# Kernel tuning notes

Hardware: AMD Instinct MI355X
Metric: run time of the kernel (lower is better)

## Reference

```python
import jax, jax.numpy as jnp
import numpy as np

NUM_MESHES = 8
NUM_FACES = 16384
NUM_NEIGHBOR = 3
SAMPLES_PER_NEIGHBOR = 8
NUM_SAMPLES = NUM_NEIGHBOR * SAMPLES_PER_NEIGHBOR  # 24
NUM_KERNEL = 64


def setup_inputs() -> dict:
    key = jax.random.key(0)
    ks = jax.random.split(key, 8)
    centers = jax.random.normal(ks[0], (NUM_MESHES, NUM_FACES, 3), dtype=jnp.float32)
    ring_n = jax.random.randint(ks[1], (NUM_MESHES, NUM_FACES, NUM_NEIGHBOR), 0, NUM_FACES)
    neighbor_corners = jax.random.normal(ks[2], (NUM_MESHES, NUM_FACES, NUM_NEIGHBOR, 3, 3), dtype=jnp.float32)
    # AlphaBetaGamma.initialize(): barycentric weights from r1, r2
    r1 = jax.random.uniform(ks[3], (NUM_FACES, NUM_SAMPLES), dtype=jnp.float32)
    r2 = jax.random.uniform(ks[4], (NUM_FACES, NUM_SAMPLES), dtype=jnp.float32)
    r1_sqrt = jnp.sqrt(r1)
    alpha = 1.0 - r1_sqrt
    beta = r1_sqrt * (1.0 - r2)
    gamma = r1_sqrt * r2
    W = jax.random.normal(ks[5], (NUM_KERNEL, 3), dtype=jnp.float32) * 0.1
    b = jnp.zeros((NUM_KERNEL,), dtype=jnp.float32)
    return {"centers": centers, "ring_n": ring_n, "neighbor_corners": neighbor_corners,
            "alpha": alpha, "beta": beta, "gamma": gamma, "W": W, "b": b}


def reference(centers, ring_n, neighbor_corners, alpha, beta, gamma, W, b):
    # Uniform neighbor resampling: tile each neighbor SAMPLES_PER_NEIGHBOR times
    # (torch.cat([neighbor_corners] * freq, dim=2))
    rs_nc = jnp.concatenate([neighbor_corners] * SAMPLES_PER_NEIGHBOR, axis=2)  # [M,F,S,3,3]
    c1, c2, c3 = rs_nc[:, :, :, 0, :], rs_nc[:, :, :, 1, :], rs_nc[:, :, :, 2, :]
    # barycentric surface points on neighbor faces: [M,F,S,3]
    a = alpha[None, :, :, None]
    bt = beta[None, :, :, None]
    g = gamma[None, :, :, None]
    points = a * c1 + bt * c2 + g * c3
    # geodesic direction vectors from face center to surface points
    dirs = points - centers[:, :, None, :]  # [M,F,S,3]
    # per-point kernel response, ReLU, then max over samples
    fea = jax.nn.relu(jnp.einsum('mfsc,kc->mfsk', dirs, W) + b)  # [M,F,S,K]
    out = jnp.max(fea, axis=2)  # [M,F,K]
    return out
```

## Files before the change

### kernel.cpp

```cpp
#include <hip/hip_runtime.h>


#define NM 8
#define NF 16384
#define NK 64

__global__ __launch_bounds__(256) void conv_surface_kernel(
    const float* __restrict__ centers,
    const float* __restrict__ nc,
    const float* __restrict__ beta,
    const float* __restrict__ gammav,
    const float* __restrict__ W,
    const float* __restrict__ b,
    float* __restrict__ out)
{
    const int lane = threadIdx.x & 63;
    const int wav  = __builtin_amdgcn_readfirstlane((int)(threadIdx.x >> 6));
    const int f    = blockIdx.x * 4 + wav;

    const float w0 = W[lane * 3 + 0];
    const float w1 = W[lane * 3 + 1];
    const float w2 = W[lane * 3 + 2];
    const float bk = b[lane];

    const float* __restrict__ bp = beta   + (size_t)f * 24;
    const float* __restrict__ gp = gammav + (size_t)f * 24;
    float bs[24], gs[24];
#pragma unroll
    for (int s = 0; s < 24; ++s) { bs[s] = bp[s]; gs[s] = gp[s]; }

#pragma unroll 2
    for (int m = 0; m < NM; ++m) {
        const size_t gidx = (size_t)m * NF + f;

        const float* __restrict__ cp = centers + gidx * 3;
        const float cdot = cp[0] * w0 + cp[1] * w1 + cp[2] * w2;

        const float* __restrict__ tp = nc + gidx * 27;
        float mx = -3.4e38f;
#pragma unroll
        for (int n = 0; n < 3; ++n) {
            const float* __restrict__ t = tp + n * 9;
            const float a1 = t[0] * w0 + t[1] * w1 + t[2] * w2;
            const float a2 = t[3] * w0 + t[4] * w1 + t[5] * w2;
            const float a3 = t[6] * w0 + t[7] * w1 + t[8] * w2;
            const float e2 = a2 - a1;
            const float e3 = a3 - a1;

            float v[8];
#pragma unroll
            for (int j = 0; j < 8; ++j) {
                const int s = n + 3 * j;
                v[j] = fmaf(bs[s], e2, fmaf(gs[s], e3, a1));
            }
            const float m0 = fmaxf(fmaxf(v[0], v[1]), fmaxf(v[2], v[3]));
            const float m1 = fmaxf(fmaxf(v[4], v[5]), fmaxf(v[6], v[7]));
            mx = fmaxf(mx, fmaxf(m0, m1));
        }

        out[gidx * NK + lane] = fmaxf(mx - cdot + bk, 0.0f);
    }
}

extern "C" void kernel_launch(void* const* d_in, const int* in_sizes, int n_in,
                              void* d_out, int out_size, void* d_ws, size_t ws_size,
                              hipStream_t stream) {
    const float* centers = (const float*)d_in[0];
    const float* nc      = (const float*)d_in[2];
    const float* beta    = (const float*)d_in[4];
    const float* gammav  = (const float*)d_in[5];
    const float* W       = (const float*)d_in[6];
    const float* b       = (const float*)d_in[7];
    float* out = (float*)d_out;

    dim3 grid(NF / 4), block(256);
    hipLaunchKernelGGL(conv_surface_kernel, grid, block, 0, stream,
                       centers, nc, beta, gammav, W, b, out);
}
```

Baseline: 36.66 us.

## Interchange mesh and neighbor loops to batch loads across all meshes

Swaps the loop order so the outer loop runs over the three neighbors and the inner loop over all eight meshes. For each neighbor, the triangle corners of every mesh are loaded together before compute, which raises memory-level parallelism. Only eight beta/gamma values per neighbor are held at a time instead of all 24, and launch bounds now request four blocks per CU. Stores are deferred to the end and need eight accumulators plus a 72-float staging array, which raises register pressure against the occupancy hint and risks spills.

```diff
diff --git a/kernel.cpp b/kernel.cpp
--- a/kernel.cpp
+++ b/kernel.cpp
@@ -5,7 +5,7 @@
 #define NF 16384
 #define NK 64
 
-__global__ __launch_bounds__(256) void conv_surface_kernel(
+__global__ __launch_bounds__(256, 4) void conv_surface_kernel(
     const float* __restrict__ centers,
     const float* __restrict__ nc,
     const float* __restrict__ beta,
@@ -23,43 +23,58 @@
     const float w2 = W[lane * 3 + 2];
     const float bk = b[lane];
 
-    const float* __restrict__ bp = beta   + (size_t)f * 24;
-    const float* __restrict__ gp = gammav + (size_t)f * 24;
-    float bs[24], gs[24];
+    float cdot[NM], mx[NM];
 #pragma unroll
-    for (int s = 0; s < 24; ++s) { bs[s] = bp[s]; gs[s] = gp[s]; }
+    for (int m = 0; m < NM; ++m) {
+        const float* __restrict__ cp = centers + ((size_t)m * NF + f) * 3;
+        cdot[m] = cp[0] * w0 + cp[1] * w1 + cp[2] * w2;
+        mx[m]   = -3.4e38f;
+    }
 
-#pragma unroll 2
-    for (int m = 0; m < NM; ++m) {
-        const size_t gidx = (size_t)m * NF + f;
+#pragma unroll
+    for (int n = 0; n < 3; ++n) {
+        float bn[8], gn[8];
+#pragma unroll
+        for (int j = 0; j < 8; ++j) {
+            bn[j] = beta  [(size_t)f * 24 + n + 3 * j];
+            gn[j] = gammav[(size_t)f * 24 + n + 3 * j];
+        }
 
-        const float* __restrict__ cp = centers + gidx * 3;
-        const float cdot = cp[0] * w0 + cp[1] * w1 + cp[2] * w2;
+        float ta[NM][9];
+#pragma unroll
+        for (int m = 0; m < NM; ++m) {
+            const float* __restrict__ t = nc + ((size_t)m * NF + f) * 27 + n * 9;
+#pragma unroll
+            for (int e = 0; e < 9; ++e) ta[m][e] = t[e];
+        }
 
-        const float* __restrict__ tp = nc + gidx * 27;
-        float mx = -3.4e38f;
 #pragma unroll
-        for (int n = 0; n < 3; ++n) {
-            const float* __restrict__ t = tp + n * 9;
-            const float a1 = t[0] * w0 + t[1] * w1 + t[2] * w2;
-            const float a2 = t[3] * w0 + t[4] * w1 + t[5] * w2;
-            const float a3 = t[6] * w0 + t[7] * w1 + t[8] * w2;
+        for (int m = 0; m < NM; ++m) {
+            const float a1 = ta[m][0] * w0 + ta[m][1] * w1 + ta[m][2] * w2;
+            const float a2 = ta[m][3] * w0 + ta[m][4] * w1 + ta[m][5] * w2;
+            const float a3 = ta[m][6] * w0 + ta[m][7] * w1 + ta[m][8] * w2;
             const float e2 = a2 - a1;
             const float e3 = a3 - a1;
 
-            float v[8];
+            const float v0 = fmaf(bn[0], e2, fmaf(gn[0], e3, a1));
+            const float v1 = fmaf(bn[1], e2, fmaf(gn[1], e3, a1));
+            const float v2 = fmaf(bn[2], e2, fmaf(gn[2], e3, a1));
+            const float v3 = fmaf(bn[3], e2, fmaf(gn[3], e3, a1));
+            const float v4 = fmaf(bn[4], e2, fmaf(gn[4], e3, a1));
+            const float v5 = fmaf(bn[5], e2, fmaf(gn[5], e3, a1));
+            const float v6 = fmaf(bn[6], e2, fmaf(gn[6], e3, a1));
+            const float v7 = fmaf(bn[7], e2, fmaf(gn[7], e3, a1));
+
+            const float p0 = fmaxf(fmaxf(v0, v1), v2);
+            const float p1 = fmaxf(fmaxf(v3, v4), v5);
+            const float p2 = fmaxf(fmaxf(v6, v7), p0);
+            mx[m] = fmaxf(mx[m], fmaxf(p1, p2));
+        }
+    }
+
 #pragma unroll
-            for (int j = 0; j < 8; ++j) {
-                const int s = n + 3 * j;
-                v[j] = fmaf(bs[s], e2, fmaf(gs[s], e3, a1));
-            }
-            const float m0 = fmaxf(fmaxf(v[0], v[1]), fmaxf(v[2], v[3]));
-            const float m1 = fmaxf(fmaxf(v[4], v[5]), fmaxf(v[6], v[7]));
-            mx = fmaxf(mx, fmaxf(m0, m1));
-        }
-
-        out[gidx * NK + lane] = fmaxf(mx - cdot + bk, 0.0f);
-    }
+    for (int m = 0; m < NM; ++m)
+        out[((size_t)m * NF + f) * NK + lane] = fmaxf(mx[m] + (bk - cdot[m]), 0.0f);
 }
 
 extern "C" void kernel_launch(void* const* d_in, const int* in_sizes, int n_in,
```

Measured after the change: 36.63 us. Within noise of the previous version (-0.1%).
